# Performance work log

Hardware: AMD Instinct MI355X
Metric: run time of the kernel (lower is better)

Reference implementation:

```python
import jax, jax.numpy as jnp
import numpy as np

N = 50000   # num nodes
E = 800000  # num edges (avg degree 16)
D = 64      # input feature dim
H = 64      # hidden dim
O = 32      # output dim


def setup_inputs() -> dict:
    key = jax.random.key(0)
    ks = jax.random.split(key, 8)
    def lin(k, fan_in, fan_out):
        # Kaiming-uniform-ish init, stored as [in, out] so forward is x @ W
        bound = 1.0 / np.sqrt(fan_in)
        return jax.random.uniform(k, (fan_in, fan_out), jnp.float32, -bound, bound)
    return {
        "x": jax.random.normal(ks[0], (N, D), jnp.float32),
        "edge_index": jax.random.randint(ks[1], (2, E), 0, N),
        "W_in1": lin(ks[2], D, H),
        "W_neigh1": lin(ks[3], D, H),
        "bias1": jnp.zeros((H,), jnp.float32),
        "W_in2": lin(ks[4], H, H),
        "W_neigh2": lin(ks[5], H, H),
        "bias2": jnp.zeros((H,), jnp.float32),
        "W_out": lin(ks[6], H, O),
        "b_out": jnp.zeros((O,), jnp.float32),
    }


def reference(x, edge_index, W_in1, W_neigh1, bias1, W_in2, W_neigh2, bias2, W_out, b_out):
    row, col = edge_index[0], edge_index[1]  # source, target
    # get_laplacian(sym) + remove_self_loops + negate -> norm = d^-1/2[row] * d^-1/2[col]
    deg = jax.ops.segment_sum(jnp.ones((E,), x.dtype), row, num_segments=N)
    dinv = jnp.where(deg > 0, deg ** -0.5, jnp.zeros((), x.dtype))
    norm = dinv[row] * dinv[col]  # [E]

    def conv(h, W_in, W_neigh, bias):
        # message: gather transformed source features, scale by per-edge norm
        msg = (h @ W_neigh)[row] * norm[:, None]          # [E, out]
        agg = jax.ops.segment_sum(msg, col, num_segments=N)  # scatter-add -> [N, out]
        return h @ W_in + agg + bias[None, :]

    h = jax.nn.relu(conv(x, W_in1, W_neigh1, bias1))
    h = jax.nn.relu(conv(h, W_in2, W_neigh2, bias2))
    return h @ W_out + b_out[None, :]  # variant='equi': per-node output [N, O]
```

## Files before the change

### kernel.cpp

```cpp
#include <hip/hip_runtime.h>
#include <hip/hip_bf16.h>


#define NCHUNK 32
#define NRANGE_H 4
#define HIST_H 12544
#define NRANGE_B 8
#define HIST_B 6272

__global__ __launch_bounds__(1024) void k_hist(const int* __restrict__ ei,
                                               int* __restrict__ partial,
                                               int N, int E, int range) {
  __shared__ int hist[HIST_H];
  int c = blockIdx.x % NCHUNK;
  int r = (blockIdx.x / NCHUNK) % NRANGE_H;
  int a = blockIdx.x / (NCHUNK * NRANGE_H);
  const int* ids = ei + (size_t)a * E;
  int lo = r * range;
  int hi = min(N, lo + range);
  int len = hi - lo;
  for (int i = threadIdx.x; i < len; i += 1024) hist[i] = 0;
  __syncthreads();
  int e0 = (int)((long long)E * c / NCHUNK);
  int e1 = (int)((long long)E * (c + 1) / NCHUNK);
  for (int e = e0 + threadIdx.x; e < e1; e += 1024) {
    int id = ids[e];
    if (id >= lo && id < hi) atomicAdd(&hist[id - lo], 1);
  }
  __syncthreads();
  int* dst = partial + ((size_t)a * NCHUNK + c) * N + lo;
  for (int i = threadIdx.x; i < len; i += 1024) dst[i] = hist[i];
}

__global__ __launch_bounds__(1024) void k_dinv_scan(const int* __restrict__ partial,
                                                    float* __restrict__ dinv,
                                                    int* __restrict__ indeg,
                                                    int* __restrict__ ptr,
                                                    int* __restrict__ bsum, int N) {
  __shared__ int s[1024];
  int g = blockIdx.x * 1024 + threadIdx.x;
  int deg = 0, ind = 0;
  if (g < N) {
#pragma unroll
    for (int c = 0; c < NCHUNK; ++c) {
      deg += partial[(size_t)c * N + g];
      ind += partial[((size_t)NCHUNK + c) * N + g];
    }
    dinv[g] = (deg > 0) ? (1.0f / sqrtf((float)deg)) : 0.0f;
    indeg[g] = ind;
  }
  s[threadIdx.x] = ind;
  __syncthreads();
  for (int off = 1; off < 1024; off <<= 1) {
    int tv = (threadIdx.x >= off) ? s[threadIdx.x - off] : 0;
    __syncthreads();
    s[threadIdx.x] += tv;
    __syncthreads();
  }
  if (g < N) ptr[g] = s[threadIdx.x] - ind;
  if (threadIdx.x == 1023) bsum[blockIdx.x] = s[1023];
}

__global__ __launch_bounds__(256) void k_base(const int* __restrict__ partial,
                                              const int* __restrict__ bsum,
                                              int* __restrict__ ptr,
                                              int* __restrict__ base, int N, int nb) {
  __shared__ int pbs[64];
  if (threadIdx.x == 0) {
    int acc = 0;
    for (int i = 0; i < nb; ++i) { pbs[i] = acc; acc += bsum[i]; }
  }
  __syncthreads();
  int n = blockIdx.x * 256 + threadIdx.x;
  if (n >= N) return;
  int run = ptr[n] + pbs[n >> 10];
  ptr[n] = run;
#pragma unroll
  for (int c = 0; c < NCHUNK; ++c) {
    base[(size_t)c * N + n] = run;
    run += partial[((size_t)NCHUNK + c) * N + n];
  }
}

__global__ __launch_bounds__(1024) void k_bin2(const int* __restrict__ ei,
                                               const int* __restrict__ base,
                                               int* __restrict__ csr_row,
                                               int N, int E, int range) {
  __shared__ int cnt[HIST_B];
  __shared__ int base_s[HIST_B];
  int c = blockIdx.x % NCHUNK;
  int r = blockIdx.x / NCHUNK;
  const int* row = ei;
  const int* col = ei + E;
  int lo = r * range;
  int hi = min(N, lo + range);
  int len = hi - lo;
  const int* bsrc = base + (size_t)c * N + lo;
  for (int i = threadIdx.x; i < len; i += 1024) {
    cnt[i] = 0;
    base_s[i] = bsrc[i];
  }
  __syncthreads();
  int e0 = (int)((long long)E * c / NCHUNK);
  int e1 = (int)((long long)E * (c + 1) / NCHUNK);
  for (int e = e0 + threadIdx.x; e < e1; e += 1024) {
    int cl = col[e];
    int rw = row[e];
    if (cl >= lo && cl < hi) {
      int off = atomicAdd(&cnt[cl - lo], 1);
      csr_row[base_s[cl - lo] + off] = rw;
    }
  }
}

template <bool RELU>
__global__ __launch_bounds__(256) void k_dual_gemm(
    const float* h,
    const float* __restrict__ Wn,
    const float* __restrict__ Wi,
    const float* __restrict__ bias,
    const float* __restrict__ dinv,
    __hip_bfloat16* __restrict__ t, float* agg, int N) {
  __shared__ float Wn_s[64 * 64];
  __shared__ float Wi_s[64 * 64];
  __shared__ float b_s[64];
  __shared__ float h_s[32 * 68];

  const int tid = threadIdx.x;
  {
    const float4* Wn4 = (const float4*)Wn;
    const float4* Wi4 = (const float4*)Wi;
    for (int i = tid; i < 1024; i += 256) {
      ((float4*)Wn_s)[i] = Wn4[i];
      ((float4*)Wi_s)[i] = Wi4[i];
    }
  }
  if (tid < 64) b_s[tid] = bias[tid];

  const int j = tid & 63;
  const int rg = tid >> 6;
  const int r0 = blockIdx.x * 64;

  for (int g = 0; g < 2; ++g) {
    __syncthreads();
    for (int v = tid; v < 512; v += 256) {
      int rr = v >> 4;
      int c4 = v & 15;
      int rload = r0 + g * 32 + rr;
      float4 val = make_float4(0.f, 0.f, 0.f, 0.f);
      if (rload < N) {
        val = *(const float4*)&h[(size_t)rload * 64 + c4 * 4];
        if (RELU) {
          val.x = fmaxf(val.x, 0.f); val.y = fmaxf(val.y, 0.f);
          val.z = fmaxf(val.z, 0.f); val.w = fmaxf(val.w, 0.f);
        }
      }
      *(float4*)&h_s[rr * 68 + c4 * 4] = val;
    }
    __syncthreads();

    float acc_t[8] = {0.f, 0.f, 0.f, 0.f, 0.f, 0.f, 0.f, 0.f};
    float acc_a[8] = {0.f, 0.f, 0.f, 0.f, 0.f, 0.f, 0.f, 0.f};
    for (int k4 = 0; k4 < 16; ++k4) {
      float4 hv[8];
#pragma unroll
      for (int r = 0; r < 8; ++r)
        hv[r] = *(const float4*)&h_s[(rg * 8 + r) * 68 + k4 * 4];
#pragma unroll
      for (int kk = 0; kk < 4; ++kk) {
        int k = k4 * 4 + kk;
        float wn = Wn_s[k * 64 + j];
        float wi = Wi_s[k * 64 + j];
#pragma unroll
        for (int r = 0; r < 8; ++r) {
          float hk = ((const float*)&hv[r])[kk];
          acc_t[r] = fmaf(hk, wn, acc_t[r]);
          acc_a[r] = fmaf(hk, wi, acc_a[r]);
        }
      }
    }
#pragma unroll
    for (int r = 0; r < 8; ++r) {
      int rr = r0 + g * 32 + rg * 8 + r;
      if (rr < N) {
        t[(size_t)rr * 64 + j] = __float2bfloat16(acc_t[r] * dinv[rr]);
        agg[(size_t)rr * 64 + j] = acc_a[r] + b_s[j];
      }
    }
  }
}

__global__ __launch_bounds__(256) void k_gather(
    const int* __restrict__ csr_row, const int* __restrict__ ptr,
    const int* __restrict__ indeg, const float* __restrict__ dinv,
    const __hip_bfloat16* __restrict__ t, float* __restrict__ agg, int N) {
  int n = blockIdx.x * 4 + (threadIdx.x >> 6);
  if (n >= N) return;
  int lane = threadIdx.x & 63;
  int q = lane >> 4;
  int fl = lane & 15;
  int i0 = ptr[n];
  int end = i0 + indeg[n];
  float dn = dinv[n];

  float4 aggv = make_float4(0.f, 0.f, 0.f, 0.f);
  if (q == 0) aggv = *(const float4*)&agg[(size_t)n * 64 + 4 * fl];

  float4 acc = make_float4(0.f, 0.f, 0.f, 0.f);
  int i = i0 + q;
  for (; i + 4 < end; i += 8) {
    int ra = csr_row[i];
    int rb = csr_row[i + 4];
    ushort4 ua = *(const ushort4*)&t[(size_t)ra * 64 + 4 * fl];
    ushort4 ub = *(const ushort4*)&t[(size_t)rb * 64 + 4 * fl];
    float4 va, vb;
    ((unsigned*)&va)[0] = (unsigned)ua.x << 16; ((unsigned*)&va)[1] = (unsigned)ua.y << 16;
    ((unsigned*)&va)[2] = (unsigned)ua.z << 16; ((unsigned*)&va)[3] = (unsigned)ua.w << 16;
    ((unsigned*)&vb)[0] = (unsigned)ub.x << 16; ((unsigned*)&vb)[1] = (unsigned)ub.y << 16;
    ((unsigned*)&vb)[2] = (unsigned)ub.z << 16; ((unsigned*)&vb)[3] = (unsigned)ub.w << 16;
    acc.x += va.x + vb.x; acc.y += va.y + vb.y;
    acc.z += va.z + vb.z; acc.w += va.w + vb.w;
  }
  for (; i < end; i += 4) {
    int ra = csr_row[i];
    ushort4 ua = *(const ushort4*)&t[(size_t)ra * 64 + 4 * fl];
    float4 va;
    ((unsigned*)&va)[0] = (unsigned)ua.x << 16; ((unsigned*)&va)[1] = (unsigned)ua.y << 16;
    ((unsigned*)&va)[2] = (unsigned)ua.z << 16; ((unsigned*)&va)[3] = (unsigned)ua.w << 16;
    acc.x += va.x; acc.y += va.y; acc.z += va.z; acc.w += va.w;
  }
  acc.x += __shfl_xor(acc.x, 16); acc.y += __shfl_xor(acc.y, 16);
  acc.z += __shfl_xor(acc.z, 16); acc.w += __shfl_xor(acc.w, 16);
  acc.x += __shfl_xor(acc.x, 32); acc.y += __shfl_xor(acc.y, 32);
  acc.z += __shfl_xor(acc.z, 32); acc.w += __shfl_xor(acc.w, 32);
  if (q == 0) {
    aggv.x += dn * acc.x; aggv.y += dn * acc.y;
    aggv.z += dn * acc.z; aggv.w += dn * acc.w;
    *(float4*)&agg[(size_t)n * 64 + 4 * fl] = aggv;
  }
}

__global__ __launch_bounds__(256) void k_gather_out(
    const int* __restrict__ csr_row, const int* __restrict__ ptr,
    const int* __restrict__ indeg, const float* __restrict__ dinv,
    const __hip_bfloat16* __restrict__ t, const float* __restrict__ agg,
    const float* __restrict__ Wo,
    const float* __restrict__ bo,
    float* __restrict__ out, int N) {
  __shared__ float Wo_s[64 * 32];
  __shared__ float bo_s[32];
  __shared__ float rowbuf[4][64];

  const int tid = threadIdx.x;
  for (int i = tid; i < 2048; i += 256) Wo_s[i] = Wo[i];
  if (tid < 32) bo_s[tid] = bo[tid];
  __syncthreads();

  int w = tid >> 6;
  int n = blockIdx.x * 4 + w;
  if (n >= N) return;
  int lane = tid & 63;
  int q = lane >> 4;
  int fl = lane & 15;
  int i0 = ptr[n];
  int end = i0 + indeg[n];
  float dn = dinv[n];

  float4 aggv = make_float4(0.f, 0.f, 0.f, 0.f);
  if (q == 0) aggv = *(const float4*)&agg[(size_t)n * 64 + 4 * fl];

  float4 acc = make_float4(0.f, 0.f, 0.f, 0.f);
  int i = i0 + q;
  for (; i + 4 < end; i += 8) {
    int ra = csr_row[i];
    int rb = csr_row[i + 4];
    ushort4 ua = *(const ushort4*)&t[(size_t)ra * 64 + 4 * fl];
    ushort4 ub = *(const ushort4*)&t[(size_t)rb * 64 + 4 * fl];
    float4 va, vb;
    ((unsigned*)&va)[0] = (unsigned)ua.x << 16; ((unsigned*)&va)[1] = (unsigned)ua.y << 16;
    ((unsigned*)&va)[2] = (unsigned)ua.z << 16; ((unsigned*)&va)[3] = (unsigned)ua.w << 16;
    ((unsigned*)&vb)[0] = (unsigned)ub.x << 16; ((unsigned*)&vb)[1] = (unsigned)ub.y << 16;
    ((unsigned*)&vb)[2] = (unsigned)ub.z << 16; ((unsigned*)&vb)[3] = (unsigned)ub.w << 16;
    acc.x += va.x + vb.x; acc.y += va.y + vb.y;
    acc.z += va.z + vb.z; acc.w += va.w + vb.w;
  }
  for (; i < end; i += 4) {
    int ra = csr_row[i];
    ushort4 ua = *(const ushort4*)&t[(size_t)ra * 64 + 4 * fl];
    float4 va;
    ((unsigned*)&va)[0] = (unsigned)ua.x << 16; ((unsigned*)&va)[1] = (unsigned)ua.y << 16;
    ((unsigned*)&va)[2] = (unsigned)ua.z << 16; ((unsigned*)&va)[3] = (unsigned)ua.w << 16;
    acc.x += va.x; acc.y += va.y; acc.z += va.z; acc.w += va.w;
  }
  acc.x += __shfl_xor(acc.x, 16); acc.y += __shfl_xor(acc.y, 16);
  acc.z += __shfl_xor(acc.z, 16); acc.w += __shfl_xor(acc.w, 16);
  acc.x += __shfl_xor(acc.x, 32); acc.y += __shfl_xor(acc.y, 32);
  acc.z += __shfl_xor(acc.z, 32); acc.w += __shfl_xor(acc.w, 32);
  if (q == 0) {
    rowbuf[w][4 * fl + 0] = fmaxf(aggv.x + dn * acc.x, 0.f);
    rowbuf[w][4 * fl + 1] = fmaxf(aggv.y + dn * acc.y, 0.f);
    rowbuf[w][4 * fl + 2] = fmaxf(aggv.z + dn * acc.z, 0.f);
    rowbuf[w][4 * fl + 3] = fmaxf(aggv.w + dn * acc.w, 0.f);
  }
  int half = lane >> 5;
  int j = lane & 31;
  float ov = 0.f;
#pragma unroll 8
  for (int k = 32 * half; k < 32 * half + 32; ++k)
    ov = fmaf(rowbuf[w][k], Wo_s[k * 32 + j], ov);
  ov += __shfl_xor(ov, 32);
  if (half == 0) out[(size_t)n * 32 + j] = ov + bo_s[j];
}

extern "C" void kernel_launch(void* const* d_in, const int* in_sizes, int n_in,
                              void* d_out, int out_size, void* d_ws, size_t ws_size,
                              hipStream_t stream) {
  const float* x = (const float*)d_in[0];
  const int* ei = (const int*)d_in[1];
  const float* W_in1 = (const float*)d_in[2];
  const float* W_neigh1 = (const float*)d_in[3];
  const float* bias1 = (const float*)d_in[4];
  const float* W_in2 = (const float*)d_in[5];
  const float* W_neigh2 = (const float*)d_in[6];
  const float* bias2 = (const float*)d_in[7];
  const float* W_out = (const float*)d_in[8];
  const float* b_out = (const float*)d_in[9];
  float* out = (float*)d_out;

  const int N = in_sizes[0] / 64;
  const int E = in_sizes[1] / 2;

  char* ws = (char*)d_ws;
  size_t off = 0;
  auto alloc = [&](size_t bytes) -> void* {
    void* p = ws + off;
    off += (bytes + 255) & ~(size_t)255;
    return p;
  };
  float* dinv = (float*)alloc((size_t)N * 4);
  int* indeg = (int*)alloc((size_t)N * 4);
  int* ptr = (int*)alloc((size_t)N * 4);
  int* bsum = (int*)alloc(256);
  int* csr_row = (int*)alloc((size_t)E * 4);
  int* partial = (int*)alloc((size_t)2 * NCHUNK * N * 4);
  int* base = (int*)alloc((size_t)NCHUNK * N * 4);
  __hip_bfloat16* t = (__hip_bfloat16*)alloc((size_t)N * 64 * 2);
  float* agg = (float*)alloc((size_t)N * 64 * 4);
  (void)ws_size;

  int range_h = (N + NRANGE_H - 1) / NRANGE_H;
  int range_b = (N + NRANGE_B - 1) / NRANGE_B;
  int gN = (N + 255) / 256;
  int gRows = (N + 63) / 64;
  int gNode = (N + 3) / 4;
  int nb = (N + 1023) / 1024;

  k_hist<<<2 * NRANGE_H * NCHUNK, 1024, 0, stream>>>(ei, partial, N, E, range_h);
  k_dinv_scan<<<nb, 1024, 0, stream>>>(partial, dinv, indeg, ptr, bsum, N);
  k_base<<<gN, 256, 0, stream>>>(partial, bsum, ptr, base, N, nb);
  k_bin2<<<NRANGE_B * NCHUNK, 1024, 0, stream>>>(ei, base, csr_row, N, E, range_b);

  k_dual_gemm<false><<<gRows, 256, 0, stream>>>(x, W_neigh1, W_in1, bias1, dinv, t, agg, N);
  k_gather<<<gNode, 256, 0, stream>>>(csr_row, ptr, indeg, dinv, t, agg, N);

  k_dual_gemm<true><<<gRows, 256, 0, stream>>>(agg, W_neigh2, W_in2, bias2, dinv, t, agg, N);
  k_gather_out<<<gNode, 256, 0, stream>>>(csr_row, ptr, indeg, dinv, t, agg,
                                          W_out, b_out, out, N);
}
```

Measured before the change: 234.4 us.

## Use bf16 MFMA for the dual per-layer GEMMs

Replaces the FP32 FMA-based dual GEMM (h@W_neigh and h@W_in) with bf16 MFMA 16x16x32 instructions. Weights are converted to bf16 in LDS, and each wave loads its 16-row A fragment directly from global memory and converts it to bf16. The goal is to cut ALU time in the GEMM stages. In exchange, the inputs and weights lose precision, including the self-term path that previously stayed in fp32.

```diff
diff --git a/kernel.cpp b/kernel.cpp
--- a/kernel.cpp
+++ b/kernel.cpp
@@ -7,6 +7,9 @@
 #define HIST_H 12544
 #define NRANGE_B 8
 #define HIST_B 6272
+
+typedef __attribute__((ext_vector_type(8))) short bfrag;
+typedef __attribute__((ext_vector_type(4))) float f32x4;
 
 __global__ __launch_bounds__(1024) void k_hist(const int* __restrict__ ei,
                                                int* __restrict__ partial,
@@ -114,77 +117,97 @@
 }
 
 template <bool RELU>
-__global__ __launch_bounds__(256) void k_dual_gemm(
+__global__ __launch_bounds__(256) void k_dual_gemm_mfma(
     const float* h,
     const float* __restrict__ Wn,
     const float* __restrict__ Wi,
     const float* __restrict__ bias,
     const float* __restrict__ dinv,
     __hip_bfloat16* __restrict__ t, float* agg, int N) {
-  __shared__ float Wn_s[64 * 64];
-  __shared__ float Wi_s[64 * 64];
+  __shared__ short Wn_s[64 * 66];
+  __shared__ short Wi_s[64 * 66];
   __shared__ float b_s[64];
-  __shared__ float h_s[32 * 68];
 
   const int tid = threadIdx.x;
-  {
-    const float4* Wn4 = (const float4*)Wn;
-    const float4* Wi4 = (const float4*)Wi;
-    for (int i = tid; i < 1024; i += 256) {
-      ((float4*)Wn_s)[i] = Wn4[i];
-      ((float4*)Wi_s)[i] = Wi4[i];
-    }
+  for (int i = tid; i < 4096; i += 256) {
+    int k = i >> 6, n = i & 63;
+    __hip_bfloat16 a = __float2bfloat16(Wn[i]);
+    __hip_bfloat16 b = __float2bfloat16(Wi[i]);
+    Wn_s[k * 66 + n] = *(short*)&a;
+    Wi_s[k * 66 + n] = *(short*)&b;
   }
   if (tid < 64) b_s[tid] = bias[tid];
-
-  const int j = tid & 63;
-  const int rg = tid >> 6;
-  const int r0 = blockIdx.x * 64;
-
-  for (int g = 0; g < 2; ++g) {
-    __syncthreads();
-    for (int v = tid; v < 512; v += 256) {
-      int rr = v >> 4;
-      int c4 = v & 15;
-      int rload = r0 + g * 32 + rr;
-      float4 val = make_float4(0.f, 0.f, 0.f, 0.f);
-      if (rload < N) {
-        val = *(const float4*)&h[(size_t)rload * 64 + c4 * 4];
-        if (RELU) {
-          val.x = fmaxf(val.x, 0.f); val.y = fmaxf(val.y, 0.f);
-          val.z = fmaxf(val.z, 0.f); val.w = fmaxf(val.w, 0.f);
-        }
+  __syncthreads();
+
+  const int lane = tid & 63;
+  const int w = tid >> 6;
+  const int m = lane & 15;
+  const int quad = lane >> 4;
+
+  bfrag Bn[4][2], Bi[4][2];
+#pragma unroll
+  for (int ct = 0; ct < 4; ++ct)
+#pragma unroll
+    for (int kb = 0; kb < 2; ++kb) {
+      bfrag vn, vi;
+#pragma unroll
+      for (int j = 0; j < 8; ++j) {
+        int k = kb * 32 + quad * 8 + j;
+        int n = ct * 16 + m;
+        vn[j] = Wn_s[k * 66 + n];
+        vi[j] = Wi_s[k * 66 + n];
       }
-      *(float4*)&h_s[rr * 68 + c4 * 4] = val;
-    }
-    __syncthreads();
-
-    float acc_t[8] = {0.f, 0.f, 0.f, 0.f, 0.f, 0.f, 0.f, 0.f};
-    float acc_a[8] = {0.f, 0.f, 0.f, 0.f, 0.f, 0.f, 0.f, 0.f};
-    for (int k4 = 0; k4 < 16; ++k4) {
-      float4 hv[8];
-#pragma unroll
-      for (int r = 0; r < 8; ++r)
-        hv[r] = *(const float4*)&h_s[(rg * 8 + r) * 68 + k4 * 4];
-#pragma unroll
-      for (int kk = 0; kk < 4; ++kk) {
-        int k = k4 * 4 + kk;
-        float wn = Wn_s[k * 64 + j];
-        float wi = Wi_s[k * 64 + j];
-#pragma unroll
-        for (int r = 0; r < 8; ++r) {
-          float hk = ((const float*)&hv[r])[kk];
-          acc_t[r] = fmaf(hk, wn, acc_t[r]);
-          acc_a[r] = fmaf(hk, wi, acc_a[r]);
-        }
+      Bn[ct][kb] = vn;
+      Bi[ct][kb] = vi;
+    }
+
+  const int r0 = blockIdx.x * 64 + w * 16;
+  const int arow = r0 + m;
+
+  bfrag A[2];
+#pragma unroll
+  for (int kb = 0; kb < 2; ++kb) {
+    bfrag av = {};
+    if (arow < N) {
+      const float* src = &h[(size_t)arow * 64 + kb * 32 + quad * 8];
+      float4 f0 = *(const float4*)src;
+      float4 f1 = *(const float4*)(src + 4);
+      float tmp[8] = {f0.x, f0.y, f0.z, f0.w, f1.x, f1.y, f1.z, f1.w};
+#pragma unroll
+      for (int j = 0; j < 8; ++j) {
+        float v = RELU ? fmaxf(tmp[j], 0.f) : tmp[j];
+        __hip_bfloat16 hb = __float2bfloat16(v);
+        av[j] = *(short*)&hb;
       }
     }
-#pragma unroll
-    for (int r = 0; r < 8; ++r) {
-      int rr = r0 + g * 32 + rg * 8 + r;
-      if (rr < N) {
-        t[(size_t)rr * 64 + j] = __float2bfloat16(acc_t[r] * dinv[rr]);
-        agg[(size_t)rr * 64 + j] = acc_a[r] + b_s[j];
+    A[kb] = av;
+  }
+
+  f32x4 accT[4], accA[4];
+#pragma unroll
+  for (int ct = 0; ct < 4; ++ct) {
+    f32x4 z = {0.f, 0.f, 0.f, 0.f};
+    accT[ct] = z;
+    accA[ct] = z;
+  }
+#pragma unroll
+  for (int ct = 0; ct < 4; ++ct) {
+    accT[ct] = __builtin_amdgcn_mfma_f32_16x16x32_bf16(A[0], Bn[ct][0], accT[ct], 0, 0, 0);
+    accT[ct] = __builtin_amdgcn_mfma_f32_16x16x32_bf16(A[1], Bn[ct][1], accT[ct], 0, 0, 0);
+    accA[ct] = __builtin_amdgcn_mfma_f32_16x16x32_bf16(A[0], Bi[ct][0], accA[ct], 0, 0, 0);
+    accA[ct] = __builtin_amdgcn_mfma_f32_16x16x32_bf16(A[1], Bi[ct][1], accA[ct], 0, 0, 0);
+  }
+
+#pragma unroll
+  for (int reg = 0; reg < 4; ++reg) {
+    int r = r0 + quad * 4 + reg;
+    if (r < N) {
+      float dv = dinv[r];
+#pragma unroll
+      for (int ct = 0; ct < 4; ++ct) {
+        int col = ct * 16 + m;
+        t[(size_t)r * 64 + col] = __float2bfloat16(accT[ct][reg] * dv);
+        agg[(size_t)r * 64 + col] = accA[ct][reg] + b_s[col];
       }
     }
   }
@@ -360,10 +383,10 @@
   k_base<<<gN, 256, 0, stream>>>(partial, bsum, ptr, base, N, nb);
   k_bin2<<<NRANGE_B * NCHUNK, 1024, 0, stream>>>(ei, base, csr_row, N, E, range_b);
 
-  k_dual_gemm<false><<<gRows, 256, 0, stream>>>(x, W_neigh1, W_in1, bias1, dinv, t, agg, N);
+  k_dual_gemm_mfma<false><<<gRows, 256, 0, stream>>>(x, W_neigh1, W_in1, bias1, dinv, t, agg, N);
   k_gather<<<gNode, 256, 0, stream>>>(csr_row, ptr, indeg, dinv, t, agg, N);
 
-  k_dual_gemm<true><<<gRows, 256, 0, stream>>>(agg, W_neigh2, W_in2, bias2, dinv, t, agg, N);
+  k_dual_gemm_mfma<true><<<gRows, 256, 0, stream>>>(agg, W_neigh2, W_in2, bias2, dinv, t, agg, N);
   k_gather_out<<<gNode, 256, 0, stream>>>(csr_row, ptr, indeg, dinv, t, agg,
                                           W_out, b_out, out, N);
 }
```

After: 204.2 us. 1.15x faster.
